# Performance work log

Measured on AMD Instinct MI355X. Metric: run time of the kernel, lower is better.

## Reference

```python
import jax, jax.numpy as jnp
from jax import lax
import numpy as np

B, S, G = 16, 384, 384
N = S + G
E_CHAR, D = 100, 128
H = D // 2              # LSTM hidden per direction
NHEAD, NHID = 4, 64
T = 21                  # crf_input_dim = label_alphabet.size() + 1
START, STOP = T - 2, T - 1
ALPHA = 0.2
CHAR_V, GAZ_V = 8000, 100000
NEG = -9e15             # pyGAT masked_fill value


def setup_inputs():
    key = jax.random.key(0)
    ks = jax.random.split(key, 20)
    f32 = jnp.float32
    def nrm(k, shape, s=0.05):
        return (jax.random.normal(k, shape) * s).astype(f32)
    eye = jnp.eye(N, dtype=bool)
    def adj(k):
        return ((jax.random.uniform(k, (B, N, N)) < 0.1) | eye[None]).astype(jnp.int32)
    return dict(
        batch_char=jax.random.randint(ks[0], (B, S), 0, CHAR_V),
        batch_len=jnp.full((B,), S, jnp.int32),
        gaz_list=jax.random.randint(ks[1], (B, G), 0, GAZ_V),
        t_graph=adj(ks[2]), c_graph=adj(ks[3]), l_graph=adj(ks[4]),
        mask=jnp.ones((B, S), jnp.int32),
        char_table=nrm(ks[5], (CHAR_V, E_CHAR)),
        gaz_table=nrm(ks[6], (GAZ_V, D)),
        w_ih_f=nrm(ks[7], (4 * H, E_CHAR)), w_hh_f=nrm(ks[8], (4 * H, H)),
        b_f=jnp.zeros((4 * H,), f32),
        w_ih_b=nrm(ks[9], (4 * H, E_CHAR)), w_hh_b=nrm(ks[10], (4 * H, H)),
        b_b=jnp.zeros((4 * H,), f32),
        h2h_W=nrm(ks[11], (T, D)), h2h_b=jnp.zeros((T,), f32),
        gat_Wh=nrm(ks[12], (3, NHEAD, D, NHID)),
        gat_ah=nrm(ks[13], (3, NHEAD, 2 * NHID)),
        gat_Wo=nrm(ks[14], (3, NHEAD * NHID, T)),
        gat_ao=nrm(ks[15], (3, 2 * T)),
        fuse_w=jnp.ones((4,), f32),
        transitions=nrm(ks[16], (T, T)),
    )


def _lstm_dir(x, w_ih, w_hh, b, reverse):
    # x: [B,S,E]; torch gate order i,f,g,o
    Bb = x.shape[0]
    Hh = w_hh.shape[1]
    xw = jnp.einsum('bse,ge->bsg', x, w_ih) + b
    def step(carry, xt):
        h, c = carry
        g = xt + h @ w_hh.T
        i, f, gg, o = jnp.split(g, 4, axis=-1)
        c = jax.nn.sigmoid(f) * c + jax.nn.sigmoid(i) * jnp.tanh(gg)
        h = jax.nn.sigmoid(o) * jnp.tanh(c)
        return (h, c), h
    h0 = jnp.zeros((Bb, Hh), x.dtype)
    _, hs = lax.scan(step, (h0, h0), xw.swapaxes(0, 1), reverse=reverse)
    return hs.swapaxes(0, 1)


def _gat_layer(x, adj, W, a, concat):
    # pyGAT batched layer: e_ij = LeakyReLU(a . [Wh_i || Wh_j]), masked softmax over j
    h = jnp.einsum('bnd,df->bnf', x, W)
    F_ = W.shape[1]
    f1 = h @ a[:F_]           # [B,N]
    f2 = h @ a[F_:]
    e = jax.nn.leaky_relu(f1[:, :, None] + f2[:, None, :], negative_slope=ALPHA)
    e = jnp.where(adj > 0, e, NEG)
    att = jax.nn.softmax(e, axis=-1)
    out = jnp.einsum('bij,bjf->bif', att, h)
    return jax.nn.elu(out) if concat else out


def _gat(x, adj, Wh, ah, Wo, ao):
    heads = jax.vmap(lambda W, a: _gat_layer(x, adj, W, a, True))(Wh, ah)  # [H,B,N,F]
    hcat = jnp.moveaxis(heads, 0, 2).reshape(x.shape[0], x.shape[1], -1)
    return jax.nn.elu(_gat_layer(hcat, adj, Wo, ao, False))


def _crf_feature(batch_char, gaz_list, graphs, char_table, gaz_table,
                 w_ih_f, w_hh_f, b_f, w_ih_b, w_hh_b, b_b, h2h_W, h2h_b,
                 gat_Wh, gat_ah, gat_Wo, gat_ao, fuse_w):
    emb = char_table[batch_char]                      # [B,S,E_CHAR]
    hf = _lstm_dir(emb, w_ih_f, w_hh_f, b_f, False)
    hb = _lstm_dir(emb, w_ih_b, w_hh_b, b_b, True)
    lstm_feat = jnp.concatenate([hf, hb], axis=-1)    # [B,S,D]
    gaz_feat = gaz_table[gaz_list]                    # [B,G,D]
    gat_in = jnp.concatenate([lstm_feat, gaz_feat], axis=1)  # [B,N,D]
    gat_outs = [_gat(gat_in, adj, gat_Wh[k], gat_ah[k], gat_Wo[k], gat_ao[k])[:, :S]
                for k, adj in enumerate(graphs)]
    lstm_proj = lstm_feat @ h2h_W.T + h2h_b           # [B,S,T]
    return (fuse_w[0] * lstm_proj + fuse_w[1] * gat_outs[0]
            + fuse_w[2] * gat_outs[1] + fuse_w[3] * gat_outs[2])


def _viterbi(feats, transitions, mask):
    Bb, Ss, Tt = feats.shape
    ids = jnp.arange(Tt)
    part0 = feats[:, 0, :] + transitions[START][None, :]
    def step(part, inp):
        feat_t, m_t = inp
        cur = part[:, :, None] + transitions[None] + feat_t[:, None, :]  # [B,prev,cur]
        new = cur.max(axis=1)
        bp = cur.argmax(axis=1)
        m = (m_t > 0)[:, None]
        return jnp.where(m, new, part), jnp.where(m, bp, ids[None, :])
    part, bps = lax.scan(step, part0,
                         (feats[:, 1:].swapaxes(0, 1), mask[:, 1:].swapaxes(0, 1)))
    last_tag = jnp.argmax(part + transitions[:, STOP][None, :], axis=1)
    def back(tag, bp):
        prev = jnp.take_along_axis(bp, tag[:, None], axis=1)[:, 0]
        return prev, prev
    _, prevs = lax.scan(back, last_tag, bps, reverse=True)   # prevs[j] = tag at time j
    return jnp.concatenate([prevs.swapaxes(0, 1), last_tag[:, None]], axis=1)


def reference(batch_char, batch_len, gaz_list, t_graph, c_graph, l_graph, mask,
              char_table, gaz_table, w_ih_f, w_hh_f, b_f, w_ih_b, w_hh_b, b_b,
              h2h_W, h2h_b, gat_Wh, gat_ah, gat_Wo, gat_ao, fuse_w, transitions):
    # batch_len is all == S (mask all ones), so packed BiLSTM == plain BiLSTM
    feats = _crf_feature(batch_char, gaz_list, (t_graph, c_graph, l_graph),
                         char_table, gaz_table, w_ih_f, w_hh_f, b_f,
                         w_ih_b, w_hh_b, b_b, h2h_W, h2h_b,
                         gat_Wh, gat_ah, gat_Wo, gat_ao, fuse_w)
    return _viterbi(feats, transitions, mask)
```

## Files before the change

kernel.cpp:

```cpp
#include <hip/hip_runtime.h>
#include <hip/hip_bf16.h>
#include <cstdint>
#include <cstddef>

#define BB 16
#define SS 384
#define GG 384
#define NN 768
#define DD 128
#define EC 100
#define TT 21
#define NHEADS 4
#define BN (BB*NN)
#define BS (BB*SS)

typedef float v2f __attribute__((ext_vector_type(2)));

__device__ __forceinline__ float sigf(float x) { return 1.0f / (1.0f + __expf(-x)); }
__device__ __forceinline__ float tanh_fast(float x) {
    return 1.0f - 2.0f / (__expf(2.0f * x) + 1.0f);
}
__device__ __forceinline__ float wred_max(float v) {
    #pragma unroll
    for (int o = 32; o > 0; o >>= 1) v = fmaxf(v, __shfl_xor(v, o));
    return v;
}
__device__ __forceinline__ float wred_sum(float v) {
    #pragma unroll
    for (int o = 32; o > 0; o >>= 1) v += __shfl_xor(v, o);
    return v;
}
__device__ __forceinline__ float rlane(float v, int l) {
    return __uint_as_float(__builtin_amdgcn_readlane(__float_as_uint(v), l));
}
__device__ __forceinline__ void gl_lds16(const float* gsrc, float* ldst) {
    __builtin_amdgcn_global_load_lds(
        (const __attribute__((address_space(1))) void*)gsrc,
        (__attribute__((address_space(3))) void*)ldst, 16, 0, 0);
}

__global__ __launch_bounds__(256) void k_xw(
    const int* __restrict__ batch_char, const float* __restrict__ char_table,
    const float* __restrict__ w_ih_f, const float* __restrict__ b_f,
    const float* __restrict__ w_ih_b, const float* __restrict__ b_b,
    float* __restrict__ xw_f, float* __restrict__ xw_b)
{
    __shared__ float At[EC * 68];
    __shared__ float Bt[EC * 68];
    __shared__ int   chs[64];
    const int tid = threadIdx.x;
    const int rt  = blockIdx.x;
    const int ot  = blockIdx.y;
    const int dir = ot >> 2, gt = ot & 3;
    const float* wih  = dir ? w_ih_b : w_ih_f;
    const float* bias = dir ? b_b    : b_f;
    float*       out  = dir ? xw_b   : xw_f;

    if (tid < 64) chs[tid] = batch_char[rt * 64 + tid];
    __syncthreads();
    for (int idx = tid; idx < 64 * EC; idx += 256) {
        int r = idx / EC, e = idx - r * EC;
        At[e * 68 + r] = char_table[(size_t)chs[r] * EC + e];
        Bt[e * 68 + r] = wih[(size_t)(gt * 64 + r) * EC + e];
    }
    __syncthreads();

    const int ty = tid >> 4, tx = tid & 15;
    const int r0 = ty * 4, c0 = tx * 4;
    float acc[4][4] = {};
    #pragma unroll 4
    for (int e = 0; e < EC; ++e) {
        float4 a = *(const float4*)&At[e * 68 + r0];
        float4 bv = *(const float4*)&Bt[e * 68 + c0];
        float av[4] = {a.x, a.y, a.z, a.w};
        float bb[4] = {bv.x, bv.y, bv.z, bv.w};
        #pragma unroll
        for (int i = 0; i < 4; ++i)
            #pragma unroll
            for (int j = 0; j < 4; ++j) acc[i][j] = fmaf(av[i], bb[j], acc[i][j]);
    }
    #pragma unroll
    for (int i = 0; i < 4; ++i) {
        int row = rt * 64 + r0 + i;
        int gc  = gt * 64 + c0;
        float4 o;
        o.x = acc[i][0] + bias[gc + 0];
        o.y = acc[i][1] + bias[gc + 1];
        o.z = acc[i][2] + bias[gc + 2];
        o.w = acc[i][3] + bias[gc + 3];
        *(float4*)&out[(size_t)row * 256 + gc] = o;
    }
}

__global__ __launch_bounds__(256) void k_gaz(
    const int* __restrict__ gaz_list, const float* __restrict__ gaz_table,
    float* __restrict__ gat_in)
{
    int idx = blockIdx.x * 256 + threadIdx.x;
    int d = idx & 127;
    int rest = idx >> 7;
    int g = rest % GG;
    int b = rest / GG;
    float v = gaz_table[(size_t)gaz_list[b * GG + g] * DD + d];
    gat_in[((size_t)b * NN + SS + g) * DD + d] = v;
}

__global__ __launch_bounds__(256, 1) void k_lstm(
    const float* __restrict__ xw_f, const float* __restrict__ xw_b,
    const float* __restrict__ w_hh_f, const float* __restrict__ w_hh_b,
    float* __restrict__ gat_in)
{
    __shared__ __align__(16) float xwc[64][256];
    __shared__ __align__(16) float hist[64][64];
    const int tid = threadIdx.x, w = tid >> 6, l = tid & 63;
    const int b = blockIdx.x >> 1, dir = blockIdx.x & 1;
    const int g = l >> 4, u = w * 16 + (l & 15);
    const float* xw  = (dir ? xw_b : xw_f) + (size_t)b * SS * 256;
    const float* whh = dir ? w_hh_b : w_hh_f;
    float* gout = gat_in + ((size_t)b * NN) * DD + dir * 64;

    v2f wr[32];
    {
        const float4* r4 = (const float4*)(whh + (size_t)(g * 64 + u) * 64);
        #pragma unroll
        for (int q = 0; q < 16; ++q) {
            float4 v = r4[q];
            wr[2 * q]     = v2f{v.x, v.y};
            wr[2 * q + 1] = v2f{v.z, v.w};
        }
    }
    if (tid < 64) hist[63][tid] = 0.f;

    {
        const int gt0 = dir ? (SS - 32) : 0;
        #pragma unroll
        for (int r = 0; r < 8; ++r) {
            int s = w * 8 + r;
            int lrow = dir ? (31 - s) : s;
            gl_lds16(xw + (size_t)(gt0 + s) * 256 + l * 4, &xwc[lrow][0]);
        }
    }
    __syncthreads();

    float c = 0.f;
    const int xoff = g * 64 + u;

    for (int tt = 0; tt < SS; ++tt) {
        if ((tt & 31) == 0) {
            const int ch = tt >> 5;
            if (ch + 1 < SS / 32) {
                const int c1 = ch + 1;
                const int gt0 = dir ? (SS - (c1 + 1) * 32) : (c1 * 32);
                #pragma unroll
                for (int r = 0; r < 8; ++r) {
                    int s = w * 8 + r;
                    int lrow = ((c1 * 32) + (dir ? (31 - s) : s)) & 63;
                    gl_lds16(xw + (size_t)(gt0 + s) * 256 + l * 4, &xwc[lrow][0]);
                }
            }
            if (ch >= 1) {
                const int cf = ch - 1;
                int i = tid >> 3;
                int col = (tid & 7) * 8;
                int row = (cf * 32 + i) & 63;
                int t = dir ? (SS - 1 - (cf * 32 + i)) : (cf * 32 + i);
                float4 v0 = *(const float4*)&hist[row][col];
                float4 v1 = *(const float4*)&hist[row][col + 4];
                *(float4*)&gout[(size_t)t * DD + col] = v0;
                *(float4*)&gout[(size_t)t * DD + col + 4] = v1;
            }
        }
        float hl = hist[(tt - 1) & 63][l];
        float x = xwc[tt & 63][xoff];
        v2f s0{0.f, 0.f}, s1{0.f, 0.f}, s2{0.f, 0.f}, s3{0.f, 0.f};
        #pragma unroll
        for (int j = 0; j < 8; ++j) {
            v2f h0{rlane(hl, 2 * j),      rlane(hl, 2 * j + 1)};
            v2f h1{rlane(hl, 2 * j + 16), rlane(hl, 2 * j + 17)};
            v2f h2{rlane(hl, 2 * j + 32), rlane(hl, 2 * j + 33)};
            v2f h3{rlane(hl, 2 * j + 48), rlane(hl, 2 * j + 49)};
            s0 = __builtin_elementwise_fma(h0, wr[j],      s0);
            s1 = __builtin_elementwise_fma(h1, wr[j + 8],  s1);
            s2 = __builtin_elementwise_fma(h2, wr[j + 16], s2);
            s3 = __builtin_elementwise_fma(h3, wr[j + 24], s3);
        }
        v2f sv = (s0 + s1) + (s2 + s3);
        float gv = sv.x + sv.y + x;
        const int srcl = l & 15;
        float gi = __shfl(gv, srcl);
        float gf = __shfl(gv, srcl + 16);
        float gg = __shfl(gv, srcl + 32);
        float go = __shfl(gv, srcl + 48);
        float nc = sigf(gf) * c + sigf(gi) * tanh_fast(gg);
        float nh = sigf(go) * tanh_fast(nc);
        c = nc;
        if (l < 16) hist[tt & 63][u] = nh;
        __syncthreads();
    }
    {
        const int cf = SS / 32 - 1;
        int i = tid >> 3;
        int col = (tid & 7) * 8;
        int row = (cf * 32 + i) & 63;
        int t = dir ? (SS - 1 - (cf * 32 + i)) : (cf * 32 + i);
        float4 v0 = *(const float4*)&hist[row][col];
        float4 v1 = *(const float4*)&hist[row][col + 4];
        *(float4*)&gout[(size_t)t * DD + col] = v0;
        *(float4*)&gout[(size_t)t * DD + col + 4] = v1;
    }
}

__global__ __launch_bounds__(256) void k_p1(
    const float* __restrict__ gat_in, const float* __restrict__ gat_Wh,
    const float* __restrict__ gat_ah, int k,
    float* __restrict__ h1, float* __restrict__ f1g, float* __restrict__ f2g)
{
    __shared__ float At[64 * 68];
    __shared__ float Bt[64 * 68];
    __shared__ float sf1[64], sf2[64];
    const int tid = threadIdx.x;
    const int rt = blockIdx.x, hd = blockIdx.y;
    if (tid < 64) { sf1[tid] = 0.f; sf2[tid] = 0.f; }
    const float* W = gat_Wh + ((size_t)(k * NHEADS + hd)) * DD * 64;
    const int ty = tid >> 4, tx = tid & 15;
    const int r0 = ty * 4, c0 = tx * 4;
    float acc[4][4] = {};
    for (int ph = 0; ph < 2; ++ph) {
        __syncthreads();
        for (int idx = tid; idx < 64 * 64; idx += 256) {
            int r = idx >> 6, e = idx & 63;
            At[e * 68 + r] = gat_in[((size_t)(rt * 64 + r)) * DD + ph * 64 + e];
            Bt[e * 68 + r] = W[(size_t)(ph * 64 + e) * 64 + r];
        }
        __syncthreads();
        #pragma unroll 4
        for (int e = 0; e < 64; ++e) {
            float4 a = *(const float4*)&At[e * 68 + r0];
            float4 bv = *(const float4*)&Bt[e * 68 + c0];
            float av[4] = {a.x, a.y, a.z, a.w};
            float bb[4] = {bv.x, bv.y, bv.z, bv.w};
            #pragma unroll
            for (int i = 0; i < 4; ++i)
                #pragma unroll
                for (int j = 0; j < 4; ++j) acc[i][j] = fmaf(av[i], bb[j], acc[i][j]);
        }
    }
    const float* ah = gat_ah + (size_t)(k * NHEADS + hd) * 128;
    float a1[4], a2[4];
    #pragma unroll
    for (int j = 0; j < 4; ++j) { a1[j] = ah[c0 + j]; a2[j] = ah[64 + c0 + j]; }
    #pragma unroll
    for (int i = 0; i < 4; ++i) {
        int n = rt * 64 + r0 + i;
        float4 o = make_float4(acc[i][0], acc[i][1], acc[i][2], acc[i][3]);
        *(float4*)&h1[((size_t)n * NHEADS + hd) * 64 + c0] = o;
        float p1 = acc[i][0] * a1[0] + acc[i][1] * a1[1] + acc[i][2] * a1[2] + acc[i][3] * a1[3];
        float p2 = acc[i][0] * a2[0] + acc[i][1] * a2[1] + acc[i][2] * a2[2] + acc[i][3] * a2[3];
        atomicAdd(&sf1[r0 + i], p1);
        atomicAdd(&sf2[r0 + i], p2);
    }
    __syncthreads();
    if (tid < 64) {
        f1g[hd * BN + rt * 64 + tid] = sf1[tid];
        f2g[hd * BN + rt * 64 + tid] = sf2[tid];
    }
}

__global__ __launch_bounds__(256) void k_attn1(
    const int* __restrict__ adj, const float* __restrict__ h1,
    const float* __restrict__ f1g, const float* __restrict__ f2g,
    float* __restrict__ out1, unsigned long long* __restrict__ packed)
{
    __shared__ int   nbr[NN];
    __shared__ float ep[NHEADS][NN];
    __shared__ unsigned long long wm[12];
    __shared__ int cntS;
    const int tid = threadIdx.x, wave = tid >> 6, lane = tid & 63;
    const int n = blockIdx.x;
    const int b = n / NN;
    #pragma unroll
    for (int it = 0; it < 3; ++it) {
        int j = it * 256 + tid;
        int a = adj[(size_t)n * NN + j];
        unsigned long long m = __ballot(a > 0);
        if (lane == 0) { wm[it * 4 + wave] = m; packed[(size_t)n * 12 + it * 4 + wave] = m; }
    }
    __syncthreads();
    if (wave == 0) {
        unsigned long long m = (lane < 12) ? wm[lane] : 0ULL;
        int pc = __popcll(m);
        int inc = pc;
        #pragma unroll
        for (int d = 1; d < 16; d <<= 1) { int t = __shfl_up(inc, d); if (lane >= d) inc += t; }
        int C = __shfl(inc, 11);
        if (lane == 0) cntS = C;
        int off = inc - pc;
        while (m) {
            int bit = __builtin_ctzll(m);
            nbr[off++] = lane * 64 + bit;
            m &= m - 1;
        }
    }
    __syncthreads();
    const int C = cntS;
    const int hd = wave;
    const float f1 = f1g[hd * BN + n];
    const float* f2p = f2g + hd * BN + b * NN;
    float mx = -3.0e38f;
    for (int t = lane; t < C; t += 64) {
        float e = f1 + f2p[nbr[t]];
        e = (e >= 0.f) ? e : 0.2f * e;
        ep[hd][t] = e;
        mx = fmaxf(mx, e);
    }
    mx = wred_max(mx);
    float sum = 0.f;
    for (int t = lane; t < C; t += 64) {
        float p = __expf(ep[hd][t] - mx);
        ep[hd][t] = p;
        sum += p;
    }
    sum = wred_sum(sum);
    const float* hb = h1 + (size_t)b * NN * (NHEADS * 64) + hd * 64 + lane;
    float ac0 = 0.f, ac1 = 0.f, ac2 = 0.f, ac3 = 0.f;
    int t = 0;
    for (; t + 3 < C; t += 4) {
        int j0 = nbr[t], j1 = nbr[t + 1], j2 = nbr[t + 2], j3 = nbr[t + 3];
        float p0 = ep[hd][t], p1 = ep[hd][t + 1], p2 = ep[hd][t + 2], p3 = ep[hd][t + 3];
        ac0 = fmaf(p0, hb[(size_t)j0 * 256], ac0);
        ac1 = fmaf(p1, hb[(size_t)j1 * 256], ac1);
        ac2 = fmaf(p2, hb[(size_t)j2 * 256], ac2);
        ac3 = fmaf(p3, hb[(size_t)j3 * 256], ac3);
    }
    for (; t < C; ++t) ac0 = fmaf(ep[hd][t], hb[(size_t)nbr[t] * 256], ac0);
    float r = ((ac0 + ac1) + (ac2 + ac3)) / sum;
    r = (r > 0.f) ? r : expm1f(r);
    out1[(size_t)n * 256 + hd * 64 + lane] = r;
}

__global__ __launch_bounds__(256) void k_p2(
    const float* __restrict__ out1, const float* __restrict__ gat_Wo,
    const float* __restrict__ gat_ao, int k,
    float* __restrict__ h2, float* __restrict__ f1o, float* __restrict__ f2o)
{
    __shared__ float ld[12 * 256];
    __shared__ float lf1[12], lf2[12];
    const int tid = threadIdx.x;
    const int blk = blockIdx.x;
    if (tid < 12) { lf1[tid] = 0.f; lf2[tid] = 0.f; }
    for (int idx = tid; idx < 12 * 256; idx += 256)
        ld[idx] = out1[(size_t)blk * 12 * 256 + idx];
    __syncthreads();
    if (tid < 252) {
        const int r = tid / TT, c = tid - r * TT;
        const float* Wo = gat_Wo + (size_t)k * 256 * TT;
        const float4* row4 = (const float4*)&ld[r * 256];
        float acc = 0.f;
        #pragma unroll 8
        for (int q4 = 0; q4 < 64; ++q4) {
            float4 v = row4[q4];
            int q = q4 * 4;
            acc = fmaf(v.x, Wo[(q + 0) * TT + c], acc);
            acc = fmaf(v.y, Wo[(q + 1) * TT + c], acc);
            acc = fmaf(v.z, Wo[(q + 2) * TT + c], acc);
            acc = fmaf(v.w, Wo[(q + 3) * TT + c], acc);
        }
        const int n = blk * 12 + r;
        h2[(size_t)n * TT + c] = acc;
        const float* ao = gat_ao + k * 2 * TT;
        atomicAdd(&lf1[r], acc * ao[c]);
        atomicAdd(&lf2[r], acc * ao[TT + c]);
    }
    __syncthreads();
    if (tid < 12) {
        f1o[blk * 12 + tid] = lf1[tid];
        f2o[blk * 12 + tid] = lf2[tid];
    }
}

__global__ __launch_bounds__(64) void k_attn2(
    const unsigned long long* __restrict__ packed,
    const float* __restrict__ h2, const float* __restrict__ f1o,
    const float* __restrict__ f2o, float* __restrict__ out2k)
{
    __shared__ int   nbr[NN];
    __shared__ float ep[NN];
    const int lane = threadIdx.x;
    const int blk = blockIdx.x;
    const int b = blk / SS, s = blk - b * SS;
    const int n = b * NN + s;
    unsigned long long w64 = (lane < 12) ? packed[(size_t)n * 12 + lane] : 0ULL;
    int pc = __popcll(w64);
    int inc = pc;
    #pragma unroll
    for (int d = 1; d < 16; d <<= 1) {
        int t = __shfl_up(inc, d, 16);
        if ((lane & 15) >= d) inc += t;
    }
    const int C = __shfl(inc, 11);
    int off = inc - pc;
    while (w64) {
        int bit = __builtin_ctzll(w64);
        nbr[off++] = lane * 64 + bit;
        w64 &= w64 - 1;
    }
    __syncthreads();
    const float f1 = f1o[n];
    const float* f2p = f2o + b * NN;
    float mx = -3.0e38f;
    for (int t = lane; t < C; t += 64) {
        int j = nbr[t];
        float e = f1 + f2p[j];
        e = (e >= 0.f) ? e : 0.2f * e;
        ep[t] = e;
        mx = fmaxf(mx, e);
    }
    mx = wred_max(mx);
    float sum = 0.f;
    for (int t = lane; t < C; t += 64) {
        float p = __expf(ep[t] - mx);
        ep[t] = p;
        sum += p;
    }
    sum = wred_sum(sum);
    const float* h2b = h2 + (size_t)b * NN * TT + ((lane < TT) ? lane : 0);
    float ac0 = 0.f, ac1 = 0.f, ac2 = 0.f, ac3 = 0.f;
    int t = 0;
    for (; t + 3 < C; t += 4) {
        int j0 = nbr[t], j1 = nbr[t + 1], j2 = nbr[t + 2], j3 = nbr[t + 3];
        float p0 = ep[t], p1 = ep[t + 1], p2 = ep[t + 2], p3 = ep[t + 3];
        ac0 = fmaf(p0, h2b[(size_t)j0 * TT], ac0);
        ac1 = fmaf(p1, h2b[(size_t)j1 * TT], ac1);
        ac2 = fmaf(p2, h2b[(size_t)j2 * TT], ac2);
        ac3 = fmaf(p3, h2b[(size_t)j3 * TT], ac3);
    }
    for (; t < C; ++t) ac0 = fmaf(ep[t], h2b[(size_t)nbr[t] * TT], ac0);
    if (lane < TT) {
        float r = ((ac0 + ac1) + (ac2 + ac3)) / sum;
        r = (r > 0.f) ? r : expm1f(r);
        out2k[(size_t)blk * TT + lane] = r;
    }
}

__global__ __launch_bounds__(64) void k_fuse(
    const float* __restrict__ gat_in, const float* __restrict__ h2h_W,
    const float* __restrict__ h2h_b, const float* __restrict__ fuse_w,
    const float* __restrict__ out2, float* __restrict__ feats)
{
    __shared__ float row[DD];
    const int lane = threadIdx.x;
    const int blk = blockIdx.x;
    const int b = blk / SS, s = blk - b * SS;
    const float* src = gat_in + ((size_t)b * NN + s) * DD;
    row[lane] = src[lane];
    row[lane + 64] = src[lane + 64];
    __syncthreads();
    if (lane < TT) {
        float acc = h2h_b[lane];
        const float4* w4 = (const float4*)&h2h_W[lane * DD];
        const float4* r4 = (const float4*)row;
        #pragma unroll 8
        for (int d4 = 0; d4 < 32; ++d4) {
            float4 w = w4[d4]; float4 v = r4[d4];
            acc = fmaf(w.x, v.x, acc); acc = fmaf(w.y, v.y, acc);
            acc = fmaf(w.z, v.z, acc); acc = fmaf(w.w, v.w, acc);
        }
        size_t o = (size_t)blk * TT + lane;
        feats[o] = fuse_w[0] * acc + fuse_w[1] * out2[o]
                 + fuse_w[2] * out2[(size_t)BS * TT + o]
                 + fuse_w[3] * out2[2 * (size_t)BS * TT + o];
    }
}

__global__ __launch_bounds__(64) void k_vit(
    const float* __restrict__ feats, const float* __restrict__ trans,
    int* __restrict__ out)
{
    __shared__ float part[24];
    __shared__ unsigned char bp[SS - 1][24];
    const int lane = threadIdx.x;
    const int b = blockIdx.x;
    const int pg = lane / TT;
    const int c = lane - pg * TT;
    const bool act = (pg < 3);
    const int p0 = pg * 7;
    float tc[7];
    if (act) {
        #pragma unroll
        for (int u = 0; u < 7; ++u) tc[u] = trans[(p0 + u) * TT + c];
    }
    if (lane < TT) part[lane] = feats[((size_t)b * SS) * TT + lane] + trans[19 * TT + lane];
    if (lane >= TT && lane < 24) part[lane] = -3.0e38f;
    __syncthreads();
    for (int t = 1; t < SS; ++t) {
        float best = -3.0e38f; int bi = 0;
        if (act) {
            #pragma unroll
            for (int u = 0; u < 7; ++u) {
                float v = part[p0 + u] + tc[u];
                if (v > best) { best = v; bi = p0 + u; }
            }
        }
        float bv1 = __shfl(best, lane + 21);
        int   bi1 = __shfl(bi,   lane + 21);
        float bv2 = __shfl(best, lane + 42);
        int   bi2 = __shfl(bi,   lane + 42);
        if (lane < TT) {
            if (bv1 > best) { best = bv1; bi = bi1; }
            if (bv2 > best) { best = bv2; bi = bi2; }
            bp[t - 1][lane] = (unsigned char)bi;
            part[lane] = best + feats[((size_t)b * SS + t) * TT + lane];
        }
        __syncthreads();
    }
    float fv = (lane < TT) ? part[lane] + trans[lane * TT + 20] : -3.0e38f;
    int fi = (lane < TT) ? lane : 0;
    #pragma unroll
    for (int o = 32; o > 0; o >>= 1) {
        float ov = __shfl_xor(fv, o);
        int oi = __shfl_xor(fi, o);
        if (ov > fv || (ov == fv && oi < fi)) { fv = ov; fi = oi; }
    }
    __syncthreads();
    if (lane == 0) {
        int cur = fi;
        out[b * SS + SS - 1] = cur;
        for (int u = SS - 2; u >= 0; --u) {
            cur = bp[u][cur];
            out[b * SS + u] = cur;
        }
    }
}

extern "C" void kernel_launch(void* const* d_in, const int* in_sizes, int n_in,
                              void* d_out, int out_size, void* d_ws, size_t ws_size,
                              hipStream_t stream) {
    (void)in_sizes; (void)n_in; (void)out_size; (void)ws_size;
    const int*   batch_char = (const int*)d_in[0];
    const int*   gaz_list   = (const int*)d_in[2];
    const int*   graphs[3]  = {(const int*)d_in[3], (const int*)d_in[4], (const int*)d_in[5]};
    const float* char_table = (const float*)d_in[7];
    const float* gaz_table  = (const float*)d_in[8];
    const float* w_ih_f = (const float*)d_in[9];
    const float* w_hh_f = (const float*)d_in[10];
    const float* b_f    = (const float*)d_in[11];
    const float* w_ih_b = (const float*)d_in[12];
    const float* w_hh_b = (const float*)d_in[13];
    const float* b_b    = (const float*)d_in[14];
    const float* h2h_W  = (const float*)d_in[15];
    const float* h2h_b  = (const float*)d_in[16];
    const float* gat_Wh = (const float*)d_in[17];
    const float* gat_ah = (const float*)d_in[18];
    const float* gat_Wo = (const float*)d_in[19];
    const float* gat_ao = (const float*)d_in[20];
    const float* fuse_w = (const float*)d_in[21];
    const float* trans  = (const float*)d_in[22];

    float* ws = (float*)d_ws;
    float* gat_in = ws;
    float* xw_f   = gat_in + 1572864;
    float* xw_b   = xw_f   + 1572864;
    float* h1     = xw_b   + 1572864;
    float* out1   = h1     + 3145728;
    float* h2     = out1   + 3145728;
    float* f1g    = h2     + 258048;
    float* f2g    = f1g    + 49152;
    float* f1o    = f2g    + 49152;
    float* f2o    = f1o    + 12288;
    float* out2   = f2o    + 12288;
    float* feats  = out2   + 387072;
    unsigned long long* packed = (unsigned long long*)(feats + 129024);

    k_xw<<<dim3(96, 8), 256, 0, stream>>>(batch_char, char_table, w_ih_f, b_f,
                                          w_ih_b, b_b, xw_f, xw_b);
    k_gaz<<<3072, 256, 0, stream>>>(gaz_list, gaz_table, gat_in);
    k_lstm<<<32, 256, 0, stream>>>(xw_f, xw_b, w_hh_f, w_hh_b, gat_in);
    for (int k = 0; k < 3; ++k) {
        k_p1<<<dim3(192, 4), 256, 0, stream>>>(gat_in, gat_Wh, gat_ah, k, h1, f1g, f2g);
        k_attn1<<<BN, 256, 0, stream>>>(graphs[k], h1, f1g, f2g, out1, packed);
        k_p2<<<1024, 256, 0, stream>>>(out1, gat_Wo, gat_ao, k, h2, f1o, f2o);
        k_attn2<<<BS, 64, 0, stream>>>(packed, h2, f1o, f2o, out2 + (size_t)k * BS * TT);
    }
    k_fuse<<<BS, 64, 0, stream>>>(gat_in, h2h_W, h2h_b, fuse_w, out2, feats);
    k_vit<<<BB, 64, 0, stream>>>(feats, trans, (int*)d_out);
}
```

Before: 966.8 us.

## Split LSTM recurrent matvec over K across waves with LDS partial-sum reduction

```diff
diff --git a/kernel.cpp b/kernel.cpp
--- a/kernel.cpp
+++ b/kernel.cpp
@@ -112,40 +112,51 @@
 {
     __shared__ __align__(16) float xwc[64][256];
     __shared__ __align__(16) float hist[64][64];
-    const int tid = threadIdx.x, w = tid >> 6, l = tid & 63;
+    __shared__ __align__(16) float part[2][4][64][4];
+    const int tid = threadIdx.x, wv = tid >> 6, l = tid & 63;
     const int b = blockIdx.x >> 1, dir = blockIdx.x & 1;
-    const int g = l >> 4, u = w * 16 + (l & 15);
     const float* xw  = (dir ? xw_b : xw_f) + (size_t)b * SS * 256;
     const float* whh = dir ? w_hh_b : w_hh_f;
     float* gout = gat_in + ((size_t)b * NN) * DD + dir * 64;
 
-    v2f wr[32];
-    {
-        const float4* r4 = (const float4*)(whh + (size_t)(g * 64 + u) * 64);
+    v2f w2[4][8];
+    #pragma unroll
+    for (int g = 0; g < 4; ++g) {
+        const float* r = whh + (size_t)(g * 64 + l) * 64 + 16 * wv;
         #pragma unroll
-        for (int q = 0; q < 16; ++q) {
-            float4 v = r4[q];
-            wr[2 * q]     = v2f{v.x, v.y};
-            wr[2 * q + 1] = v2f{v.z, v.w};
-        }
-    }
-    if (tid < 64) hist[63][tid] = 0.f;
+        for (int jj = 0; jj < 8; ++jj) w2[g][jj] = v2f{r[2 * jj], r[2 * jj + 1]};
+    }
+    const int sbase = __builtin_amdgcn_readfirstlane((tid >> 6) << 4);
 
     {
         const int gt0 = dir ? (SS - 32) : 0;
         #pragma unroll
         for (int r = 0; r < 8; ++r) {
-            int s = w * 8 + r;
+            int s = wv * 8 + r;
             int lrow = dir ? (31 - s) : s;
             gl_lds16(xw + (size_t)(gt0 + s) * 256 + l * 4, &xwc[lrow][0]);
         }
     }
     __syncthreads();
 
-    float c = 0.f;
-    const int xoff = g * 64 + u;
+    float h = 0.f, c = 0.f;
+    int buf = 0;
 
     for (int tt = 0; tt < SS; ++tt) {
+        v2f a0{0.f, 0.f}, a1{0.f, 0.f}, a2{0.f, 0.f}, a3{0.f, 0.f};
+        #pragma unroll
+        for (int jj = 0; jj < 8; ++jj) {
+            v2f hv{rlane(h, sbase + 2 * jj), rlane(h, sbase + 2 * jj + 1)};
+            a0 = __builtin_elementwise_fma(hv, w2[0][jj], a0);
+            a1 = __builtin_elementwise_fma(hv, w2[1][jj], a1);
+            a2 = __builtin_elementwise_fma(hv, w2[2][jj], a2);
+            a3 = __builtin_elementwise_fma(hv, w2[3][jj], a3);
+        }
+        float4 pw;
+        pw.x = a0.x + a0.y; pw.y = a1.x + a1.y;
+        pw.z = a2.x + a2.y; pw.w = a3.x + a3.y;
+        *(float4*)part[buf][wv][l] = pw;
+        __syncthreads();
         if ((tt & 31) == 0) {
             const int ch = tt >> 5;
             if (ch + 1 < SS / 32) {
@@ -153,7 +164,7 @@
                 const int gt0 = dir ? (SS - (c1 + 1) * 32) : (c1 * 32);
                 #pragma unroll
                 for (int r = 0; r < 8; ++r) {
-                    int s = w * 8 + r;
+                    int s = wv * 8 + r;
                     int lrow = ((c1 * 32) + (dir ? (31 - s) : s)) & 63;
                     gl_lds16(xw + (size_t)(gt0 + s) * 256 + l * 4, &xwc[lrow][0]);
                 }
@@ -170,33 +181,26 @@
                 *(float4*)&gout[(size_t)t * DD + col + 4] = v1;
             }
         }
-        float hl = hist[(tt - 1) & 63][l];
-        float x = xwc[tt & 63][xoff];
-        v2f s0{0.f, 0.f}, s1{0.f, 0.f}, s2{0.f, 0.f}, s3{0.f, 0.f};
-        #pragma unroll
-        for (int j = 0; j < 8; ++j) {
-            v2f h0{rlane(hl, 2 * j),      rlane(hl, 2 * j + 1)};
-            v2f h1{rlane(hl, 2 * j + 16), rlane(hl, 2 * j + 17)};
-            v2f h2{rlane(hl, 2 * j + 32), rlane(hl, 2 * j + 33)};
-            v2f h3{rlane(hl, 2 * j + 48), rlane(hl, 2 * j + 49)};
-            s0 = __builtin_elementwise_fma(h0, wr[j],      s0);
-            s1 = __builtin_elementwise_fma(h1, wr[j + 8],  s1);
-            s2 = __builtin_elementwise_fma(h2, wr[j + 16], s2);
-            s3 = __builtin_elementwise_fma(h3, wr[j + 24], s3);
-        }
-        v2f sv = (s0 + s1) + (s2 + s3);
-        float gv = sv.x + sv.y + x;
-        const int srcl = l & 15;
-        float gi = __shfl(gv, srcl);
-        float gf = __shfl(gv, srcl + 16);
-        float gg = __shfl(gv, srcl + 32);
-        float go = __shfl(gv, srcl + 48);
+        float4 p0 = *(const float4*)part[buf][0][l];
+        float4 p1 = *(const float4*)part[buf][1][l];
+        float4 p2 = *(const float4*)part[buf][2][l];
+        float4 p3 = *(const float4*)part[buf][3][l];
+        const int row = tt & 63;
+        float x0 = xwc[row][l];
+        float x1 = xwc[row][64 + l];
+        float x2 = xwc[row][128 + l];
+        float x3 = xwc[row][192 + l];
+        float gi = ((p0.x + p1.x) + (p2.x + p3.x)) + x0;
+        float gf = ((p0.y + p1.y) + (p2.y + p3.y)) + x1;
+        float gg = ((p0.z + p1.z) + (p2.z + p3.z)) + x2;
+        float go = ((p0.w + p1.w) + (p2.w + p3.w)) + x3;
         float nc = sigf(gf) * c + sigf(gi) * tanh_fast(gg);
-        float nh = sigf(go) * tanh_fast(nc);
+        h = sigf(go) * tanh_fast(nc);
         c = nc;
-        if (l < 16) hist[tt & 63][u] = nh;
-        __syncthreads();
-    }
+        if (wv == 0) hist[row][l] = h;
+        buf ^= 1;
+    }
+    __syncthreads();
     {
         const int cf = SS / 32 - 1;
         int i = tid >> 3;
```

Measured after the change: 968.5 us. About the same (+0.2%).
